# Optimization experiments

Hardware: AMD Instinct MI355X
Metric: run time of the kernel (lower is better)

The kernel has to match this reference:

```python
import jax, jax.numpy as jnp
import numpy as np
from jax import lax

VOX_DIMS = (9, 9, 9)
VOX = 9 * 9 * 9  # 729 voxels per sample


def setup_inputs() -> dict:
    rng = np.random.default_rng(0)
    N, B = 1_000_000, 32
    Cin, Fd, Cout = 3, 64, 64
    # per-point voxel index in the flat batched grid [0, B*VOX)
    voxel = rng.integers(0, B * VOX, size=N)
    unique, inverse = np.unique(voxel, return_inverse=True)

    key = jax.random.key(0)
    ks = jax.random.split(key, 12)
    s = 0.1
    inp = {
        "x": jax.random.normal(ks[0], (N, Cin), jnp.float32),
        "lin0_w": jax.random.normal(ks[1], (Cin, Fd), jnp.float32) * s,
        "lin0_b": jax.random.normal(ks[2], (Fd,), jnp.float32) * s,
        "conv0_w": jax.random.normal(ks[3], (Fd, Cin, 3, 3, 3), jnp.float32) * s,
        "conv0_b": jax.random.normal(ks[4], (Fd,), jnp.float32) * s,
        "lin1_w": jax.random.normal(ks[5], (Fd, Cout), jnp.float32) * s,
        "lin1_b": jax.random.normal(ks[6], (Cout,), jnp.float32) * s,
        "conv1_w": jax.random.normal(ks[7], (Cout, Fd, 3, 3, 3), jnp.float32) * s,
        "conv1_b": jax.random.normal(ks[8], (Cout,), jnp.float32) * s,
        "linf_w": jax.random.normal(ks[9], (Cin, Cout), jnp.float32) * s,
        "linf_b": jax.random.normal(ks[10], (Cout,), jnp.float32) * s,
        "consecutive_cluster": jnp.asarray(inverse, jnp.int32),
        "cluster_non_consecutive": jnp.asarray(voxel, jnp.int32),
        "unique_cluster_non_consecutive": jnp.asarray(unique, jnp.int32),
        "batch_size": B,
    }
    return inp


def _elm(x, lin_w, lin_b, conv_w, conv_b, consec, cnc, unc, B):
    """One EquivariantLinearMapsModule forward (use_attention is forced False)."""
    Cin = x.shape[1]
    Cout = lin_w.shape[1]
    inner = x @ lin_w + lin_b  # [N, Cout]

    U = unc.shape[0]
    sums = jax.ops.segment_sum(x, consec, num_segments=U)           # [U, Cin]
    counts = jax.ops.segment_sum(jnp.ones((x.shape[0], 1), x.dtype), consec, num_segments=U)
    means = sums / counts                                           # scatter_mean

    # grid[:, unique] = means.T ; then raw view to (B, Cin, 9, 9, 9) as in torch
    grid = jnp.zeros((Cin, B * VOX), x.dtype).at[:, unc].set(means.T)
    grid = grid.reshape((B, Cin) + VOX_DIMS)
    out = lax.conv_general_dilated(
        grid, conv_w, window_strides=(1, 1, 1), padding=[(1, 1)] * 3,
        dimension_numbers=("NCDHW", "OIDHW", "NCDHW"))
    out = out + conv_b[None, :, None, None, None]
    # raw view back to (Cout, B*VOX) then gather per point
    outer = out.reshape(Cout, -1)[:, cnc].T  # [N, Cout]
    return inner + outer


def reference(x, lin0_w, lin0_b, conv0_w, conv0_b, lin1_w, lin1_b, conv1_w, conv1_b,
              linf_w, linf_b, consecutive_cluster, cluster_non_consecutive,
              unique_cluster_non_consecutive, batch_size):
    x0 = x
    h = _elm(x0, lin0_w, lin0_b, conv0_w, conv0_b,
             consecutive_cluster, cluster_non_consecutive,
             unique_cluster_non_consecutive, batch_size)
    h = _elm(h, lin1_w, lin1_b, conv1_w, conv1_b,
             consecutive_cluster, cluster_non_consecutive,
             unique_cluster_non_consecutive, batch_size)
    # input_nc (3) < output_nc (64): residual via lin_first
    return h + (x0 @ linf_w + linf_b)
```

## Files before the change

### kernel.cpp

```cpp
#include <hip/hip_runtime.h>
#include <hip/hip_bf16.h>
#include <stdint.h>

typedef __hip_bfloat16 bf16;
typedef _Float16 half_t;
typedef _Float16 half8 __attribute__((ext_vector_type(8)));
typedef float f32x4 __attribute__((ext_vector_type(4)));
typedef unsigned short us8 __attribute__((ext_vector_type(8)));

#define BVOXN 23328

__device__ __forceinline__ float b2f(bf16 v) { return __bfloat162float(v); }

#define OFF_L0W   64
#define OFF_B0    256
#define OFF_W0    320
#define OFF_CB0   5504
#define OFF_L1W   5568
#define OFF_B1    9664
#define OFF_CB1   120320
#define OFF_LFW   120384
#define OFF_BF    120576
#define OFF_SUMS  120640
#define OFF_GA0   213952
#define OFF_GT    283936
#define OFF_C0T   1030432
#define OFF_WT    1776928
#define OFF_WC    1834272
#define OFF_BVEC  1834464
#define OFF_G     1834528

#define FP_SCALE 1048576.0f
#define FP_BIAS  8388608

__global__ void k_probe(const void* lin1_w, int* flag) {
    __shared__ int cnt[256];
    int t = threadIdx.x;
    const bf16* p = (const bf16*)lin1_w;
    int c = 0;
    for (int j = t; j < 2048; j += 256) {
        float v = b2f(p[2 * j]);
        if (!(v == v) || fabsf(v) > 64.0f || (v != 0.0f && fabsf(v) < 1e-20f)) c++;
    }
    cnt[t] = c;
    __syncthreads();
    for (int s = 128; s > 0; s >>= 1) {
        if (t < s) cnt[t] += cnt[t + s];
        __syncthreads();
    }
    if (t == 0) *flag = (cnt[0] > 100) ? 1 : 0;
}

__device__ __forceinline__ float ldf(const void* p, int j, int isf) {
    return isf ? ((const float*)p)[j] : b2f(((const bf16*)p)[j]);
}

#define SETUP_N 120256
__global__ void k_setup(const void* l0w, const void* l0b, const void* w0,
                        const void* cb0, const void* l1w, const void* l1b,
                        const void* w1, const void* cb1, const void* lfw,
                        const void* lfb, const int* flag, float* ws,
                        half_t* Wt, float* Wc, float* bvec) {
    int isf = *flag;
    int t = blockIdx.x * 256 + threadIdx.x;
    if (t < SETUP_N) {
        if (t < 5568) {
            const void* src;
            int j;
            float* dst;
            if (t < 192)       { src = l0w; j = t;         dst = ws + OFF_L0W + j; }
            else if (t < 256)  { src = l0b; j = t - 192;   dst = ws + OFF_B0  + j; }
            else if (t < 5440) {
                j = t - 256;
                int o = j / 81, r = j % 81, i = r / 27, tap = r % 27;
                src = w0;
                dst = ws + OFF_W0 + (i * 27 + tap) * 64 + o;
            }
            else if (t < 5504) { src = cb0; j = t - 5440;  dst = ws + OFF_CB0 + j; }
            else               { src = cb1; j = t - 5504;  dst = ws + OFF_CB1 + j; }
            *dst = ldf(src, j, isf);
        } else {
            int q = t - 5568;
            int tap = q >> 12;
            int r = q & 4095;
            int o = r >> 6, i = r & 63;
            float v;
            if (tap < 27) v = ldf(w1, (o * 64 + i) * 27 + tap, isf);
            else          v = ldf(l1w, i * 64 + o, isf);
            Wt[q] = (half_t)v;
        }
        return;
    }
    if (blockIdx.x == (SETUP_N + 255) / 256 && threadIdx.x < 64) {
        int c = threadIdx.x;
        float bv = ldf(l1b, c, isf) + ldf(lfb, c, isf);
        for (int k = 0; k < 64; ++k)
            bv += ldf(l0b, k, isf) * ldf(l1w, k * 64 + c, isf);
        bvec[c] = bv;
        for (int r = 0; r < 3; ++r) {
            float wv = ldf(lfw, r * 64 + c, isf);
            for (int k = 0; k < 64; ++k)
                wv += ldf(l0w, r * 64 + k, isf) * ldf(l1w, k * 64 + c, isf);
            Wc[r * 64 + c] = wv;
        }
    }
}

__global__ void k_accum(const void* x, const int* consec, const int* flag,
                        unsigned long long* sums8, int N) {
    int i = blockIdx.x * 256 + threadIdx.x;
    if (i >= N) return;
    int isf = *flag;
    int u = consec[i];
    float v0 = ldf(x, 3 * i + 0, isf);
    float v1 = ldf(x, 3 * i + 1, isf);
    float v2 = ldf(x, 3 * i + 2, isf);
    unsigned e0 = (unsigned)(__float2int_rn(v0 * FP_SCALE) + FP_BIAS);
    unsigned e1 = (unsigned)(__float2int_rn(v1 * FP_SCALE) + FP_BIAS);
    unsigned e2 = (unsigned)(__float2int_rn(v2 * FP_SCALE) + FP_BIAS);
    atomicAdd(&sums8[2 * u + 0], ((unsigned long long)e0 << 32) | e1);
    atomicAdd(&sums8[2 * u + 1], (1ull << 32) | e2);
}

__device__ __forceinline__ void decode_mean(const unsigned long long* sums8, int u,
                                            float& m0, float& m1, float& m2) {
    unsigned long long S1 = sums8[2 * u + 0];
    unsigned long long S2 = sums8[2 * u + 1];
    double n = (double)(unsigned)(S2 >> 32);
    double k = 1.0 / (1048576.0 * n);
    double nb = n * 8388608.0;
    m0 = (float)(((double)(unsigned)(S1 >> 32) - nb) * k);
    m1 = (float)(((double)(unsigned)(S1 & 0xffffffffu) - nb) * k);
    m2 = (float)(((double)(unsigned)(S2 & 0xffffffffu) - nb) * k);
}

__global__ void k_scatter0(const unsigned long long* sums8, const int* unc,
                           float* gridA0, int U) {
    int u = blockIdx.x * 256 + threadIdx.x;
    if (u >= U) return;
    int v = unc[u];
    float m0, m1, m2;
    decode_mean(sums8, u, m0, m1, m2);
    gridA0[0 * BVOXN + v] = m0;
    gridA0[1 * BVOXN + v] = m1;
    gridA0[2 * BVOXN + v] = m2;
}

__global__ __launch_bounds__(256) void k_conv0s(const float* gridA0, const float* w0t,
                                                const float* cb0, half_t* conv0oT) {
    __shared__ float slab[3 * 363];
    int b = blockIdx.x / 9, d = blockIdx.x % 9;
    int t = threadIdx.x;
    for (int s = t; s < 3 * 363; s += 256) {
        int i = s / 363, rr = s % 363;
        int zz = rr / 121, p = rr % 121;
        int ph = p / 11, pw = p % 11;
        int z = d + zz - 1, hh = ph - 1, ww = pw - 1;
        float v = 0.0f;
        if ((unsigned)z < 9u && (unsigned)hh < 9u && (unsigned)ww < 9u)
            v = gridA0[b * 2187 + i * 729 + z * 81 + hh * 9 + ww];
        slab[s] = v;
    }
    __syncthreads();

    int og = t >> 5, l = t & 31;
    int hw[3], hj[3], wj[3];
    bool valid[3];
    #pragma unroll
    for (int j = 0; j < 3; ++j) {
        int q = l + 32 * j;
        valid[j] = q < 81;
        int qc = q < 81 ? q : 80;
        hw[j] = q; hj[j] = qc / 9; wj[j] = qc % 9;
    }
    float acc[8][3];
    #pragma unroll
    for (int oj = 0; oj < 8; ++oj) {
        float bv = cb0[og * 8 + oj];
        acc[oj][0] = bv; acc[oj][1] = bv; acc[oj][2] = bv;
    }

    for (int i = 0; i < 3; ++i) {
        const float* sb = slab + i * 363;
        const float* wb = w0t + (i * 27) * 64 + og * 8;
        for (int kd = 0; kd < 3; ++kd)
            for (int kh = 0; kh < 3; ++kh) {
                int ib0 = kd * 121 + (hj[0] + kh) * 11 + wj[0];
                int ib1 = kd * 121 + (hj[1] + kh) * 11 + wj[1];
                int ib2 = kd * 121 + (hj[2] + kh) * 11 + wj[2];
                #pragma unroll
                for (int kw = 0; kw < 3; ++kw) {
                    int tap = kd * 9 + kh * 3 + kw;
                    const float4* w4 = reinterpret_cast<const float4*>(wb + tap * 64);
                    float4 wA = w4[0];
                    float4 wB = w4[1];
                    float in0 = sb[ib0 + kw];
                    float in1 = sb[ib1 + kw];
                    float in2 = sb[ib2 + kw];
                    acc[0][0] += wA.x * in0; acc[0][1] += wA.x * in1; acc[0][2] += wA.x * in2;
                    acc[1][0] += wA.y * in0; acc[1][1] += wA.y * in1; acc[1][2] += wA.y * in2;
                    acc[2][0] += wA.z * in0; acc[2][1] += wA.z * in1; acc[2][2] += wA.z * in2;
                    acc[3][0] += wA.w * in0; acc[3][1] += wA.w * in1; acc[3][2] += wA.w * in2;
                    acc[4][0] += wB.x * in0; acc[4][1] += wB.x * in1; acc[4][2] += wB.x * in2;
                    acc[5][0] += wB.y * in0; acc[5][1] += wB.y * in1; acc[5][2] += wB.y * in2;
                    acc[6][0] += wB.z * in0; acc[6][1] += wB.z * in1; acc[6][2] += wB.z * in2;
                    acc[7][0] += wB.w * in0; acc[7][1] += wB.w * in1; acc[7][2] += wB.w * in2;
                }
            }
    }

    #pragma unroll
    for (int oj = 0; oj < 8; ++oj) {
        int o = og * 8 + oj;
        int kraw = 2 * b + (o >> 5);
        int bvr = o & 31;
        #pragma unroll
        for (int j = 0; j < 3; ++j)
            if (valid[j])
                conv0oT[(bvr * 729 + d * 81 + hw[j]) * 64 + kraw] =
                    (half_t)acc[oj][j];
    }
}

__global__ __launch_bounds__(256) void k_scatter1(const unsigned long long* sums8,
                                                  const int* unc,
                                                  const half_t* conv0oT,
                                                  const float* l0w, const float* l0b,
                                                  half_t* gridTc, int U) {
    int u = blockIdx.x * 4 + (threadIdx.x >> 6);
    if (u >= U) return;
    int c = threadIdx.x & 63;
    int v = unc[u];
    int bvr = v / 729, pos = v % 729;
    float m0, m1, m2;
    decode_mean(sums8, u, m0, m1, m2);
    float val = l0b[c] + m0 * l0w[c] + m1 * l0w[64 + c] + m2 * l0w[128 + c] +
                (float)conv0oT[v * 64 + c];
    gridTc[((c >> 1) * 729 + pos) * 64 + ((c & 1) * 32 + bvr)] = (half_t)val;
}

__global__ __launch_bounds__(384) void k_conv1m(const half_t* __restrict__ gridTc,
                                                const half_t* __restrict__ Wt,
                                                const float* __restrict__ cb1,
                                                bf16* __restrict__ G) {
    __shared__ __align__(16) half_t slab[363 * 72];
    int bid = blockIdx.x;
    int nh = bid & 1;
    int t2 = bid >> 1;
    int b = t2 / 9, z = t2 % 9;
    int tid = threadIdx.x;

    for (int s = tid; s < 2904; s += 384) {
        int pos = s >> 3, ic = s & 7;
        int zz = pos / 121, rr = pos % 121;
        int ph = rr / 11, pw = rr % 11;
        int zi = z + zz - 1, yi = ph - 1, xi = pw - 1;
        half8 v;
        #pragma unroll
        for (int j = 0; j < 8; ++j) v[j] = (half_t)0.f;
        if ((unsigned)zi < 9u && (unsigned)yi < 9u && (unsigned)xi < 9u)
            v = *(const half8*)&gridTc[(b * 729 + zi * 81 + yi * 9 + xi) * 64 + ic * 8];
        *(half8*)&slab[pos * 72 + ic * 8] = v;
    }
    __syncthreads();

    int w = tid >> 6;
    int l = tid & 63;
    int m16 = l & 15, kb = l >> 4;
    int qbase = w * 16;
    int qa = qbase + m16; if (qa > 80) qa = 80;
    int ya = qa / 9, xa = qa % 9;
    int laneA = (ya * 11 + xa) * 72 + kb * 8;
    int o0 = nh * 32 + m16;
    f32x4 acc0 = {0.f, 0.f, 0.f, 0.f};
    f32x4 acc1 = {0.f, 0.f, 0.f, 0.f};

    const half_t* wbase = Wt + (o0 * 64 + kb * 8);

    #pragma unroll
    for (int kd = 0; kd < 3; ++kd)
      #pragma unroll
      for (int kh = 0; kh < 3; ++kh)
        #pragma unroll
        for (int kw = 0; kw < 3; ++kw) {
            int tap = kd * 9 + kh * 3 + kw;
            int sb = laneA + (kd * 121 + kh * 11 + kw) * 72;
            const half_t* wt = wbase + tap * 4096;
            #pragma unroll
            for (int is = 0; is < 2; ++is) {
                half8 a  = *(const half8*)&slab[sb + is * 32];
                half8 b0 = *(const half8*)&wt[is * 32];
                half8 b1 = *(const half8*)&wt[1024 + is * 32];
                acc0 = __builtin_amdgcn_mfma_f32_16x16x32_f16(a, b0, acc0, 0, 0, 0);
                acc1 = __builtin_amdgcn_mfma_f32_16x16x32_f16(a, b1, acc1, 0, 0, 0);
            }
        }

    float c0 = cb1[o0], c1 = cb1[o0 + 16];
    int cG = 2 * b + nh;
    int vb0 = m16 * 729 + z * 81;
    int vb1 = (m16 + 16) * 729 + z * 81;
    #pragma unroll
    for (int r = 0; r < 4; ++r) {
        int q = qbase + kb * 4 + r;
        if (q < 81) {
            G[(vb0 + q) * 64 + cG] = __float2bfloat16(acc0[r] + c0);
            G[(vb1 + q) * 64 + cG] = __float2bfloat16(acc1[r] + c1);
        }
    }
}

__global__ __launch_bounds__(256) void k_G2(const half_t* __restrict__ conv0oT,
                                            const half_t* __restrict__ Wt,
                                            bf16* __restrict__ G) {
    int wid = (blockIdx.x * 256 + threadIdx.x) >> 6;
    int v0 = wid * 16;
    if (v0 >= BVOXN) return;
    int l = threadIdx.x & 63;
    int m16 = l & 15, kb = l >> 4;
    const half_t* wt27 = Wt + 27 * 4096;
    f32x4 acc[4];
    #pragma unroll
    for (int ct = 0; ct < 4; ++ct) acc[ct] = {0.f, 0.f, 0.f, 0.f};
    const half_t* ap = conv0oT + (v0 + m16) * 64 + kb * 8;
    #pragma unroll
    for (int is = 0; is < 2; ++is) {
        half8 a = *(const half8*)&ap[is * 32];
        #pragma unroll
        for (int ct = 0; ct < 4; ++ct) {
            half8 bf = *(const half8*)&wt27[(ct * 16 + m16) * 64 + kb * 8 + is * 32];
            acc[ct] = __builtin_amdgcn_mfma_f32_16x16x32_f16(a, bf, acc[ct], 0, 0, 0);
        }
    }
    #pragma unroll
    for (int ct = 0; ct < 4; ++ct)
        #pragma unroll
        for (int r = 0; r < 4; ++r) {
            int v = v0 + kb * 4 + r;
            int c = ct * 16 + m16;
            int idx = v * 64 + c;
            G[idx] = __float2bfloat16(b2f(G[idx]) + acc[ct][r]);
        }
}

__device__ __forceinline__ unsigned short f2bf_raw(float f) {
    bf16 h = __float2bfloat16(f);
    unsigned short u;
    __builtin_memcpy(&u, &h, 2);
    return u;
}

__global__ __launch_bounds__(256) void k_out(const void* x, const int* cnc,
                                             const float* Wc, const float* bvec,
                                             const bf16* G, const int* flag,
                                             void* out, int N) {
    int t = blockIdx.x * 256 + threadIdx.x;
    int i = t >> 3;
    if (i >= N) return;
    int c8 = (t & 7) * 8;
    int isf = *flag;
    int v = cnc[i];
    float x0 = ldf(x, 3 * i + 0, isf);
    float x1 = ldf(x, 3 * i + 1, isf);
    float x2 = ldf(x, 3 * i + 2, isf);
    us8 g = *(const us8*)&G[v * 64 + c8];
    f32x4 w0a = *(const f32x4*)&Wc[c8];
    f32x4 w0b = *(const f32x4*)&Wc[c8 + 4];
    f32x4 w1a = *(const f32x4*)&Wc[64 + c8];
    f32x4 w1b = *(const f32x4*)&Wc[64 + c8 + 4];
    f32x4 w2a = *(const f32x4*)&Wc[128 + c8];
    f32x4 w2b = *(const f32x4*)&Wc[128 + c8 + 4];
    f32x4 bva = *(const f32x4*)&bvec[c8];
    f32x4 bvb = *(const f32x4*)&bvec[c8 + 4];
    f32x4 ra, rb;
    #pragma unroll
    for (int j = 0; j < 4; ++j) {
        float gfa = __uint_as_float((unsigned)g[j] << 16);
        float gfb = __uint_as_float((unsigned)g[j + 4] << 16);
        ra[j] = bva[j] + x0 * w0a[j] + x1 * w1a[j] + x2 * w2a[j] + gfa;
        rb[j] = bvb[j] + x0 * w0b[j] + x1 * w1b[j] + x2 * w2b[j] + gfb;
    }
    size_t oi = (size_t)i * 64 + c8;
    if (isf) {
        *(f32x4*)((float*)out + oi) = ra;
        *(f32x4*)((float*)out + oi + 4) = rb;
    } else {
        us8 h;
        #pragma unroll
        for (int j = 0; j < 4; ++j) {
            h[j] = f2bf_raw(ra[j]);
            h[j + 4] = f2bf_raw(rb[j]);
        }
        *(us8*)((bf16*)out + oi) = h;
    }
}

extern "C" void kernel_launch(void* const* d_in, const int* in_sizes, int n_in,
                              void* d_out, int out_size, void* d_ws, size_t ws_size,
                              hipStream_t stream) {
    const void* x       = d_in[0];
    const void* lin0_w  = d_in[1];
    const void* lin0_b  = d_in[2];
    const void* conv0_w = d_in[3];
    const void* conv0_b = d_in[4];
    const void* lin1_w  = d_in[5];
    const void* lin1_b  = d_in[6];
    const void* conv1_w = d_in[7];
    const void* conv1_b = d_in[8];
    const void* linf_w  = d_in[9];
    const void* linf_b  = d_in[10];
    const int* consec   = (const int*)d_in[11];
    const int* cnc      = (const int*)d_in[12];
    const int* unc      = (const int*)d_in[13];

    int N = in_sizes[0] / 3;
    int U = in_sizes[13];

    float* ws   = (float*)d_ws;
    int*   flag = (int*)d_ws;
    unsigned long long* sums8 = (unsigned long long*)(ws + OFF_SUMS);
    float*  gridA0  = ws + OFF_GA0;
    half_t* gridTc  = (half_t*)(ws + OFF_GT);
    half_t* conv0oT = (half_t*)(ws + OFF_C0T);
    half_t* Wt      = (half_t*)(ws + OFF_WT);
    float*  Wc      = ws + OFF_WC;
    float*  bvec    = ws + OFF_BVEC;
    bf16*   G       = (bf16*)(ws + OFF_G);

    hipMemsetAsync((char*)d_ws + (size_t)OFF_SUMS * 4, 0,
                   (size_t)(OFF_C0T - OFF_SUMS) * 4, stream);

    k_probe<<<1, 256, 0, stream>>>(lin1_w, flag);
    k_setup<<<(SETUP_N + 255) / 256 + 1, 256, 0, stream>>>(
        lin0_w, lin0_b, conv0_w, conv0_b, lin1_w, lin1_b, conv1_w, conv1_b,
        linf_w, linf_b, flag, ws, Wt, Wc, bvec);
    k_accum<<<(N + 255) / 256, 256, 0, stream>>>(x, consec, flag, sums8, N);
    k_scatter0<<<(U + 255) / 256, 256, 0, stream>>>(sums8, unc, gridA0, U);
    k_conv0s<<<288, 256, 0, stream>>>(gridA0, ws + OFF_W0, ws + OFF_CB0, conv0oT);
    k_scatter1<<<(U + 3) / 4, 256, 0, stream>>>(sums8, unc, conv0oT, ws + OFF_L0W,
                                                ws + OFF_B0, gridTc, U);
    k_conv1m<<<576, 384, 0, stream>>>(gridTc, Wt, ws + OFF_CB1, G);
    k_G2<<<(BVOXN / 16 * 64 + 255) / 256, 256, 0, stream>>>(conv0oT, Wt, G);
    long long tot = (long long)N * 8;
    k_out<<<(int)((tot + 255) / 256), 256, 0, stream>>>(x, cnc, Wc, bvec, G, flag,
                                                        d_out, N);
}
```

Measured before the change: 552.2 us.

## Merge setup with accumulation and make grid1 a dense per-voxel gather

Folds the weight-setup kernel and the atomic point-accumulation kernel into one launch, with separate block ranges for each job, which removes a launch and lets the two overlap. Scatter0 now also writes a dense per-voxel mean array with an occupancy flag. The scatter1 kernel is replaced by a dense grid kernel that covers every voxel and writes gridTc with coalesced stores, so the memset of gridTc is no longer needed. The cost is extra work on empty voxels and a larger workspace layout.

```diff
diff --git a/kernel.cpp b/kernel.cpp
--- a/kernel.cpp
+++ b/kernel.cpp
@@ -16,19 +16,16 @@
 #define OFF_B0    256
 #define OFF_W0    320
 #define OFF_CB0   5504
-#define OFF_L1W   5568
-#define OFF_B1    9664
 #define OFF_CB1   120320
-#define OFF_LFW   120384
-#define OFF_BF    120576
 #define OFF_SUMS  120640
 #define OFF_GA0   213952
-#define OFF_GT    283936
-#define OFF_C0T   1030432
-#define OFF_WT    1776928
-#define OFF_WC    1834272
-#define OFF_BVEC  1834464
-#define OFF_G     1834528
+#define OFF_MEX   283936
+#define OFF_GT    377248
+#define OFF_C0T   1123744
+#define OFF_WT    1870240
+#define OFF_WC    1927584
+#define OFF_BVEC  1927776
+#define OFF_G     1927840
 
 #define FP_SCALE 1048576.0f
 #define FP_BIAS  8388608
@@ -56,20 +53,37 @@
 }
 
 #define SETUP_N 120256
-__global__ void k_setup(const void* l0w, const void* l0b, const void* w0,
-                        const void* cb0, const void* l1w, const void* l1b,
-                        const void* w1, const void* cb1, const void* lfw,
-                        const void* lfb, const int* flag, float* ws,
-                        half_t* Wt, float* Wc, float* bvec) {
+__global__ void k_sa(const void* x, const int* consec, int N, int NA,
+                     const void* l0w, const void* l0b, const void* w0,
+                     const void* cb0, const void* l1w, const void* l1b,
+                     const void* w1, const void* cb1, const void* lfw,
+                     const void* lfb, const int* flag, float* ws,
+                     half_t* Wt, float* Wc, float* bvec,
+                     unsigned long long* sums8) {
     int isf = *flag;
-    int t = blockIdx.x * 256 + threadIdx.x;
+    int bid = blockIdx.x;
+    if (bid < NA) {
+        int i = bid * 256 + threadIdx.x;
+        if (i >= N) return;
+        int u = consec[i];
+        float v0 = ldf(x, 3 * i + 0, isf);
+        float v1 = ldf(x, 3 * i + 1, isf);
+        float v2 = ldf(x, 3 * i + 2, isf);
+        unsigned e0 = (unsigned)(__float2int_rn(v0 * FP_SCALE) + FP_BIAS);
+        unsigned e1 = (unsigned)(__float2int_rn(v1 * FP_SCALE) + FP_BIAS);
+        unsigned e2 = (unsigned)(__float2int_rn(v2 * FP_SCALE) + FP_BIAS);
+        atomicAdd(&sums8[2 * u + 0], ((unsigned long long)e0 << 32) | e1);
+        atomicAdd(&sums8[2 * u + 1], (1ull << 32) | e2);
+        return;
+    }
+    int t = (bid - NA) * 256 + threadIdx.x;
     if (t < SETUP_N) {
         if (t < 5568) {
             const void* src;
             int j;
             float* dst;
             if (t < 192)       { src = l0w; j = t;         dst = ws + OFF_L0W + j; }
-            else if (t < 256)  { src = l0b; j = t - 192;   dst = ws + OFF_B0  + j; }
+            else if (t < 256)  { src = l0b; j = t - 192;   dst = ws + 256 + (j = t - 192, j); }
             else if (t < 5440) {
                 j = t - 256;
                 int o = j / 81, r = j % 81, i = r / 27, tap = r % 27;
@@ -78,6 +92,7 @@
             }
             else if (t < 5504) { src = cb0; j = t - 5440;  dst = ws + OFF_CB0 + j; }
             else               { src = cb1; j = t - 5504;  dst = ws + OFF_CB1 + j; }
+            if (t >= 192 && t < 256) { src = l0b; j = t - 192; dst = ws + OFF_B0 + j; }
             *dst = ldf(src, j, isf);
         } else {
             int q = t - 5568;
@@ -91,7 +106,7 @@
         }
         return;
     }
-    if (blockIdx.x == (SETUP_N + 255) / 256 && threadIdx.x < 64) {
+    if (bid == NA + (SETUP_N + 255) / 256 && threadIdx.x < 64) {
         int c = threadIdx.x;
         float bv = ldf(l1b, c, isf) + ldf(lfb, c, isf);
         for (int k = 0; k < 64; ++k)
@@ -106,22 +121,6 @@
     }
 }
 
-__global__ void k_accum(const void* x, const int* consec, const int* flag,
-                        unsigned long long* sums8, int N) {
-    int i = blockIdx.x * 256 + threadIdx.x;
-    if (i >= N) return;
-    int isf = *flag;
-    int u = consec[i];
-    float v0 = ldf(x, 3 * i + 0, isf);
-    float v1 = ldf(x, 3 * i + 1, isf);
-    float v2 = ldf(x, 3 * i + 2, isf);
-    unsigned e0 = (unsigned)(__float2int_rn(v0 * FP_SCALE) + FP_BIAS);
-    unsigned e1 = (unsigned)(__float2int_rn(v1 * FP_SCALE) + FP_BIAS);
-    unsigned e2 = (unsigned)(__float2int_rn(v2 * FP_SCALE) + FP_BIAS);
-    atomicAdd(&sums8[2 * u + 0], ((unsigned long long)e0 << 32) | e1);
-    atomicAdd(&sums8[2 * u + 1], (1ull << 32) | e2);
-}
-
 __device__ __forceinline__ void decode_mean(const unsigned long long* sums8, int u,
                                             float& m0, float& m1, float& m2) {
     unsigned long long S1 = sums8[2 * u + 0];
@@ -135,7 +134,7 @@
 }
 
 __global__ void k_scatter0(const unsigned long long* sums8, const int* unc,
-                           float* gridA0, int U) {
+                           float* gridA0, f32x4* meanex, int U) {
     int u = blockIdx.x * 256 + threadIdx.x;
     if (u >= U) return;
     int v = unc[u];
@@ -144,6 +143,8 @@
     gridA0[0 * BVOXN + v] = m0;
     gridA0[1 * BVOXN + v] = m1;
     gridA0[2 * BVOXN + v] = m2;
+    f32x4 m = {m0, m1, m2, 1.0f};
+    meanex[v] = m;
 }
 
 __global__ __launch_bounds__(256) void k_conv0s(const float* gridA0, const float* w0t,
@@ -222,21 +223,22 @@
     }
 }
 
-__global__ __launch_bounds__(256) void k_scatter1(const unsigned long long* sums8,
-                                                  const int* unc,
-                                                  const half_t* conv0oT,
-                                                  const float* l0w, const float* l0b,
-                                                  half_t* gridTc, int U) {
-    int u = blockIdx.x * 4 + (threadIdx.x >> 6);
-    if (u >= U) return;
-    int c = threadIdx.x & 63;
-    int v = unc[u];
-    int bvr = v / 729, pos = v % 729;
-    float m0, m1, m2;
-    decode_mean(sums8, u, m0, m1, m2);
-    float val = l0b[c] + m0 * l0w[c] + m1 * l0w[64 + c] + m2 * l0w[128 + c] +
-                (float)conv0oT[v * 64 + c];
-    gridTc[((c >> 1) * 729 + pos) * 64 + ((c & 1) * 32 + bvr)] = (half_t)val;
+__global__ __launch_bounds__(256) void k_grid1(const f32x4* __restrict__ meanex,
+                                               const half_t* __restrict__ conv0oT,
+                                               const float* __restrict__ l0w,
+                                               const float* __restrict__ l0b,
+                                               half_t* __restrict__ gridTc) {
+    int r = blockIdx.x * 4 + (threadIdx.x >> 6);
+    int ch = threadIdx.x & 63;
+    int bp = r / 729, pos = r % 729;
+    int c = 2 * bp + (ch >> 5);
+    int v = (ch & 31) * 729 + pos;
+    f32x4 m = meanex[v];
+    float val = 0.0f;
+    if (m[3] != 0.0f)
+        val = l0b[c] + m[0] * l0w[c] + m[1] * l0w[64 + c] + m[2] * l0w[128 + c] +
+              (float)conv0oT[v * 64 + c];
+    gridTc[r * 64 + ch] = (half_t)val;
 }
 
 __global__ __launch_bounds__(384) void k_conv1m(const half_t* __restrict__ gridTc,
@@ -420,6 +422,7 @@
     int*   flag = (int*)d_ws;
     unsigned long long* sums8 = (unsigned long long*)(ws + OFF_SUMS);
     float*  gridA0  = ws + OFF_GA0;
+    f32x4*  meanex  = (f32x4*)(ws + OFF_MEX);
     half_t* gridTc  = (half_t*)(ws + OFF_GT);
     half_t* conv0oT = (half_t*)(ws + OFF_C0T);
     half_t* Wt      = (half_t*)(ws + OFF_WT);
@@ -428,17 +431,18 @@
     bf16*   G       = (bf16*)(ws + OFF_G);
 
     hipMemsetAsync((char*)d_ws + (size_t)OFF_SUMS * 4, 0,
-                   (size_t)(OFF_C0T - OFF_SUMS) * 4, stream);
+                   (size_t)(OFF_GT - OFF_SUMS) * 4, stream);
 
     k_probe<<<1, 256, 0, stream>>>(lin1_w, flag);
-    k_setup<<<(SETUP_N + 255) / 256 + 1, 256, 0, stream>>>(
+    int NA = (N + 255) / 256;
+    int SB = (SETUP_N + 255) / 256 + 1;
+    k_sa<<<NA + SB, 256, 0, stream>>>(x, consec, N, NA,
         lin0_w, lin0_b, conv0_w, conv0_b, lin1_w, lin1_b, conv1_w, conv1_b,
-        linf_w, linf_b, flag, ws, Wt, Wc, bvec);
-    k_accum<<<(N + 255) / 256, 256, 0, stream>>>(x, consec, flag, sums8, N);
-    k_scatter0<<<(U + 255) / 256, 256, 0, stream>>>(sums8, unc, gridA0, U);
+        linf_w, linf_b, flag, ws, Wt, Wc, bvec, sums8);
+    k_scatter0<<<(U + 255) / 256, 256, 0, stream>>>(sums8, unc, gridA0, meanex, U);
     k_conv0s<<<288, 256, 0, stream>>>(gridA0, ws + OFF_W0, ws + OFF_CB0, conv0oT);
-    k_scatter1<<<(U + 3) / 4, 256, 0, stream>>>(sums8, unc, conv0oT, ws + OFF_L0W,
-                                                ws + OFF_B0, gridTc, U);
+    k_grid1<<<BVOXN / 4, 256, 0, stream>>>(meanex, conv0oT, ws + OFF_L0W,
+                                           ws + OFF_B0, gridTc);
     k_conv1m<<<576, 384, 0, stream>>>(gridTc, Wt, ws + OFF_CB1, G);
     k_G2<<<(BVOXN / 16 * 64 + 255) / 256, 256, 0, stream>>>(conv0oT, Wt, G);
     long long tot = (long long)N * 8;
```

After: 546.4 us. About the same (-1.0%).
